# Optimization experiments

Measured on AMD Instinct MI355X. Metric: run time of the kernel, lower is better.

The kernel has to match this reference:

```python
import jax, jax.numpy as jnp
import numpy as np

HID, SD, EXP, DTR = 1024, 16, 2048, 64
B_, T_ = 4, 2048


def setup_inputs() -> dict:
    key = jax.random.key(0)
    ks = jax.random.split(key, 9)
    def rn(k, shape, s=0.02):
        return jax.random.normal(k, shape, jnp.float32) * s
    return {
        "x": jax.random.normal(ks[0], (B_, T_, HID), jnp.float32),
        "ln_g": jnp.ones((HID,), jnp.float32),
        "ln_b": jnp.zeros((HID,), jnp.float32),
        "W_in": rn(ks[1], (HID, 2 * EXP)),
        "b_in": jnp.zeros((2 * EXP,), jnp.float32),
        "W_del": rn(ks[2], (EXP, DTR)),
        "b_del": jnp.zeros((DTR,), jnp.float32),
        "W_dt": rn(ks[3], (DTR, EXP)),
        "b_dt": jnp.zeros((EXP,), jnp.float32),
        "W_B": rn(ks[4], (EXP, SD)),
        "b_B": jnp.zeros((SD,), jnp.float32),
        "W_C": rn(ks[5], (EXP, SD)),
        "b_C": jnp.zeros((SD,), jnp.float32),
        "A_log": -jnp.exp(0.1 * jax.random.normal(ks[6], (EXP, SD), jnp.float32)),
        "Dp": jnp.zeros((EXP,), jnp.float32),
        "W_out": rn(ks[7], (EXP, HID)),
        "b_out": jnp.zeros((HID,), jnp.float32),
    }


def _layernorm(x, g, b, eps=1e-5):
    m = jnp.mean(x, axis=-1, keepdims=True)
    v = jnp.var(x, axis=-1, keepdims=True)
    return (x - m) * jax.lax.rsqrt(v + eps) * g + b


def _selective_scan(u, delta, A, Bm, Cm):
    # u, delta: (B,T,E); Bm, Cm: (B,T,Sd); A: (E,Sd)
    def step(h, inp):
        u_t, d_t, B_t, C_t = inp  # (B,E),(B,E),(B,Sd),(B,Sd)
        A_disc = jnp.exp(d_t[..., None] * A[None])          # (B,E,Sd)
        h = A_disc * h + d_t[..., None] * B_t[:, None, :] * u_t[..., None]
        y_t = jnp.einsum("bs,bds->bd", C_t, h)
        return h, y_t
    h0 = jnp.zeros((u.shape[0], u.shape[2], A.shape[1]), u.dtype)
    xs = (u.transpose(1, 0, 2), delta.transpose(1, 0, 2),
          Bm.transpose(1, 0, 2), Cm.transpose(1, 0, 2))
    _, ys = jax.lax.scan(step, h0, xs)  # ys: (T,B,E)
    return ys.transpose(1, 0, 2)


def reference(x, ln_g, ln_b, W_in, b_in, W_del, b_del, W_dt, b_dt,
              W_B, b_B, W_C, b_C, A_log, Dp, W_out, b_out):
    res = x
    xn = _layernorm(x, ln_g, ln_b)
    xp = xn @ W_in + b_in                 # (B,T,2E)
    u, gate = jnp.split(xp, 2, axis=-1)   # each (B,T,E)
    u = jax.nn.silu(u)
    delta = jax.nn.softplus((u @ W_del + b_del) @ W_dt + b_dt)  # (B,T,E)
    Bm = u @ W_B + b_B                    # (B,T,Sd)
    Cm = u @ W_C + b_C                    # (B,T,Sd)
    A = -jnp.exp(A_log)                   # (E,Sd)
    y = _selective_scan(u, delta, A, Bm, Cm)
    y = y + u * Dp
    y = y * jax.nn.silu(gate)
    return y @ W_out + b_out + res
```

## Files before the change

kernel.cpp:

```cpp
#include <hip/hip_runtime.h>

#define HIDN 1024
#define EXPN 2048
#define SDIM 16
#define DTRN 64
#define BBN  4
#define TTN  2048
#define MMN  (BBN*TTN)
#define NCHUNK 64
#define CLEN (TTN/NCHUNK)
#define KSPL 4
#define KCH  (EXPN/KSPL)

typedef unsigned short u16;
typedef __bf16 bf16x8 __attribute__((ext_vector_type(8)));
typedef float f32x4 __attribute__((ext_vector_type(4)));
typedef float f32x2v __attribute__((ext_vector_type(2)));

static __device__ __forceinline__ float b2f(u16 u) {
    union { unsigned int i; float f; } cv; cv.i = ((unsigned int)u) << 16; return cv.f;
}
static __device__ __forceinline__ u16 f2b(float f) {
    union { float f; unsigned int i; } cv; cv.f = f;
    unsigned int x = cv.i;
    return (u16)((x + 0x7fffu + ((x >> 16) & 1u)) >> 16);
}
static __device__ __forceinline__ float fexp2(float x) {
    return __builtin_amdgcn_exp2f(x);
}
static __device__ __forceinline__ float fsilu(float v) {
    return v / (1.f + fexp2(-1.44269504088896f * v));
}
template<int L> static __device__ __forceinline__ void waitcnt_vm() {
    if constexpr (L == 0) asm volatile("s_waitcnt vmcnt(0)" ::: "memory");
    else if constexpr (L == 3) asm volatile("s_waitcnt vmcnt(3)" ::: "memory");
    else if constexpr (L == 4) asm volatile("s_waitcnt vmcnt(4)" ::: "memory");
}

static __device__ __forceinline__
void tr_tile(const float* __restrict__ W, u16* __restrict__ Wt,
             int K, int N, int bk, int bn, float (*t)[65]) {
    const int r0 = threadIdx.x >> 4, c0 = (threadIdx.x & 15) << 2;
    #pragma unroll
    for (int i = 0; i < 4; ++i) {
        float4 v = *(const float4*)(W + (size_t)(bk + r0 + i * 16) * N + bn + c0);
        t[r0 + i * 16][c0 + 0] = v.x; t[r0 + i * 16][c0 + 1] = v.y;
        t[r0 + i * 16][c0 + 2] = v.z; t[r0 + i * 16][c0 + 3] = v.w;
    }
    __syncthreads();
    #pragma unroll
    for (int i = 0; i < 4; ++i) {
        const int n = r0 + i * 16;
        ushort4 o;
        o.x = f2b(t[c0 + 0][n]); o.y = f2b(t[c0 + 1][n]);
        o.z = f2b(t[c0 + 2][n]); o.w = f2b(t[c0 + 3][n]);
        *(ushort4*)(Wt + (size_t)(bn + n) * K + bk + c0) = o;
    }
}

__global__ __launch_bounds__(256)
void k_prep(const float* __restrict__ x, const float* __restrict__ ln_g,
            const float* __restrict__ ln_b,
            const float* __restrict__ W_in, const float* __restrict__ W_out,
            const float* __restrict__ W_dt, const float* __restrict__ W_del,
            const float* __restrict__ W_B, const float* __restrict__ W_C,
            const float* __restrict__ A_log,
            u16* __restrict__ xn,
            u16* __restrict__ Wt_in, u16* __restrict__ Wt_out,
            u16* __restrict__ Wdt_t, u16* __restrict__ Wcat,
            float* __restrict__ A2) {
    __shared__ float t[64][65];
    __shared__ float as[4], bs[4];
    int blk = blockIdx.x;
    if (blk < MMN) {
        const int row = blk, tid = threadIdx.x;
        const float4 xv = ((const float4*)(x + (size_t)row * HIDN))[tid];
        float s  = xv.x + xv.y + xv.z + xv.w;
        float ss = fmaf(xv.x, xv.x, fmaf(xv.y, xv.y, fmaf(xv.z, xv.z, xv.w * xv.w)));
        #pragma unroll
        for (int o = 32; o > 0; o >>= 1) { s += __shfl_down(s, o); ss += __shfl_down(ss, o); }
        const int wid = tid >> 6, lane = tid & 63;
        if (lane == 0) { as[wid] = s; bs[wid] = ss; }
        __syncthreads();
        const float S  = as[0] + as[1] + as[2] + as[3];
        const float SS = bs[0] + bs[1] + bs[2] + bs[3];
        const float mean = S * (1.f / HIDN);
        const float var  = SS * (1.f / HIDN) - mean * mean;
        const float r = rsqrtf(var + 1e-5f);
        const float4 gv = ((const float4*)ln_g)[tid];
        const float4 bv = ((const float4*)ln_b)[tid];
        ushort4 o;
        o.x = f2b((xv.x - mean) * r * gv.x + bv.x);
        o.y = f2b((xv.y - mean) * r * gv.y + bv.y);
        o.z = f2b((xv.z - mean) * r * gv.z + bv.z);
        o.w = f2b((xv.w - mean) * r * gv.w + bv.w);
        ((ushort4*)(xn + (size_t)row * HIDN))[tid] = o;
        return;
    }
    blk -= MMN;
    if (blk < 1024) {
        tr_tile(W_in, Wt_in, HIDN, 2 * EXPN, (blk >> 6) << 6, (blk & 63) << 6, t);
        return;
    }
    blk -= 1024;
    if (blk < 512) {
        tr_tile(W_out, Wt_out, EXPN, HIDN, (blk >> 4) << 6, (blk & 15) << 6, t);
        return;
    }
    blk -= 512;
    if (blk < 32) {
        tr_tile(W_dt, Wdt_t, DTRN, EXPN, 0, blk << 6, t);
        return;
    }
    blk -= 32;
    if (blk < 768) {
        const int i = blk * 256 + threadIdx.x;
        const int n = i >> 11, k = i & 2047;
        float v;
        if (n < 64)      v = W_del[(size_t)k * DTRN + n];
        else if (n < 80) v = W_B[(size_t)k * SDIM + (n - 64)];
        else             v = W_C[(size_t)k * SDIM + (n - 80)];
        Wcat[i] = f2b(v);
        return;
    }
    blk -= 768;
    {
        const int i = blk * 256 + threadIdx.x;
        A2[i] = -__expf(A_log[i]) * 1.44269504088896340736f;
    }
}

#define MEPI_SPLIT_SILU 0
#define MEPI_OUT        1
#define MEPI_SP         2

template<int BN>
static __device__ __forceinline__
void stage256(const u16* __restrict__ A, const u16* __restrict__ Bt,
              u16 (*seg)[8192], int brow, int bcol, int K, int k0,
              int srow, int scol, int tid) {
    #pragma unroll
    for (int h = 0; h < 2; ++h) {
        const u16* sa = A + (size_t)(brow + h * 128 + srow) * K + k0 + scol;
        __builtin_amdgcn_global_load_lds(
            (const __attribute__((address_space(1))) void*)sa,
            (__attribute__((address_space(3))) void*)&seg[h][tid * 8], 16, 0, 0);
    }
    #pragma unroll
    for (int h = 0; h < BN / 128; ++h) {
        const u16* sb = Bt + (size_t)(bcol + h * 128 + srow) * K + k0 + scol;
        __builtin_amdgcn_global_load_lds(
            (const __attribute__((address_space(1))) void*)sb,
            (__attribute__((address_space(3))) void*)&seg[2 + h][tid * 8], 16, 0, 0);
    }
}

template<int BN, int EPI>
__global__ __launch_bounds__(1024)
void mgemm256(const u16* __restrict__ A, const u16* __restrict__ Bt,
              const float* __restrict__ bias, void* __restrict__ O0,
              void* __restrict__ O1, const float* __restrict__ res,
              int N, int K) {
    constexpr int NSEG = 2 + BN / 128;
    constexpr int L    = NSEG;
    constexpr int NFRag = BN / 64;
    __shared__ u16 lds[2][NSEG][8192];
    const int tid  = threadIdx.x;
    const int lane = tid & 63, wid = tid >> 6;
    const int wm = wid >> 2, wn = wid & 3;
    const int r  = lane & 15, kh = lane >> 4;
    const int brow = blockIdx.y * 256, bcol = blockIdx.x * BN;

    int srow, scol;
    {
        const int q = tid;
        const int sub = q >> 6, qi = q & 63;
        const int qis = qi ^ (((qi >> 5) & 1) << 1);
        srow = (sub >> 1) * 16 + (qi >> 2);
        scol = ((sub & 1) << 5) + (qis & 3) * 8;
    }
    const int swz_kh = kh ^ (((r >> 3) & 1) << 1);
    const int rbase  = r * 32 + swz_kh * 8;
    const int am = wm & 1;

    f32x4 acc[4][NFRag];
    #pragma unroll
    for (int i = 0; i < 4; ++i)
        #pragma unroll
        for (int n = 0; n < NFRag; ++n) acc[i][n] = (f32x4){0.f, 0.f, 0.f, 0.f};

    const int NT = K >> 6;
    stage256<BN>(A, Bt, lds[0], brow, bcol, K, 0, srow, scol, tid);
    if (NT > 1) {
        stage256<BN>(A, Bt, lds[1], brow, bcol, K, 64, srow, scol, tid);
        waitcnt_vm<L>();
    } else {
        waitcnt_vm<0>();
    }
    __builtin_amdgcn_s_barrier();
    asm volatile("" ::: "memory");

    for (int kt = 0; kt < NT; ++kt) {
        const u16* segA = lds[kt & 1][wm >> 1];
        #pragma unroll
        for (int kk = 0; kk < 2; ++kk) {
            bf16x8 a[4], b[NFRag];
            #pragma unroll
            for (int mf = 0; mf < 4; ++mf)
                a[mf] = *(const bf16x8*)&segA[((am * 4 + mf) * 2 + kk) * 512 + rbase];
            #pragma unroll
            for (int nf = 0; nf < NFRag; ++nf) {
                const int nb = wn * NFRag + nf;
                const u16* segB = lds[kt & 1][2 + (nb >> 3)];
                b[nf] = *(const bf16x8*)&segB[(((nb & 7)) * 2 + kk) * 512 + rbase];
            }
            __builtin_amdgcn_s_setprio(1);
            #pragma unroll
            for (int mf = 0; mf < 4; ++mf)
                #pragma unroll
                for (int nf = 0; nf < NFRag; ++nf)
                    acc[mf][nf] = __builtin_amdgcn_mfma_f32_16x16x32_bf16(a[mf], b[nf], acc[mf][nf], 0, 0, 0);
            __builtin_amdgcn_s_setprio(0);
        }
        __builtin_amdgcn_s_barrier(); asm volatile("" ::: "memory");
        if (kt + 2 < NT) {
            stage256<BN>(A, Bt, lds[kt & 1], brow, bcol, K, (kt + 2) * 64, srow, scol, tid);
            waitcnt_vm<L>();
        } else {
            waitcnt_vm<0>();
        }
        __builtin_amdgcn_s_barrier(); asm volatile("" ::: "memory");
    }

    const int orow = brow + wm * 64 + kh * 4;
    const int ocol = bcol + wn * (BN / 4) + r;
    if constexpr (EPI == MEPI_SPLIT_SILU) {
        u16* dst; int cb;
        if (bcol < EXPN) { dst = (u16*)O0; cb = ocol; }
        else             { dst = (u16*)O1; cb = ocol - EXPN; }
        #pragma unroll
        for (int Mf = 0; Mf < 4; ++Mf)
            #pragma unroll
            for (int Nf = 0; Nf < NFRag; ++Nf)
                #pragma unroll
                for (int j = 0; j < 4; ++j) {
                    const int row = orow + Mf * 16 + j;
                    const int col = ocol + Nf * 16;
                    float v = acc[Mf][Nf][j] + bias[col];
                    dst[(size_t)row * EXPN + cb + Nf * 16] = f2b(fsilu(v));
                }
    } else if constexpr (EPI == MEPI_SP) {
        u16* o = (u16*)O0;
        #pragma unroll
        for (int Mf = 0; Mf < 4; ++Mf)
            #pragma unroll
            for (int Nf = 0; Nf < NFRag; ++Nf)
                #pragma unroll
                for (int j = 0; j < 4; ++j) {
                    const int row = orow + Mf * 16 + j;
                    const int col = ocol + Nf * 16;
                    float v = acc[Mf][Nf][j] + bias[col];
                    float sp = (v > 20.f) ? v
                             : 0.69314718056f * __builtin_amdgcn_logf(
                                   1.f + fexp2(1.44269504089f * v));
                    o[(size_t)row * N + col] = f2b(sp);
                }
    } else {
        float* o = (float*)O0;
        #pragma unroll
        for (int Mf = 0; Mf < 4; ++Mf)
            #pragma unroll
            for (int Nf = 0; Nf < NFRag; ++Nf)
                #pragma unroll
                for (int j = 0; j < 4; ++j) {
                    const int row = orow + Mf * 16 + j;
                    const int col = ocol + Nf * 16;
                    o[(size_t)row * N + col] = acc[Mf][Nf][j] + bias[col] + res[(size_t)row * N + col];
                }
    }
}

__global__ __launch_bounds__(256)
void k_proj(const u16* __restrict__ A, const u16* __restrict__ Wcat,
            float* __restrict__ Ppart) {
    __shared__ u16 As[128 * 32];
    __shared__ u16 Bs[96 * 32];
    const int tid  = threadIdx.x;
    const int wave = tid >> 6, lane = tid & 63;
    const int brow = blockIdx.y * 128;
    const int ks   = blockIdx.x;
    const int r = lane & 15, kh = lane >> 4;

    f32x4 acc[2][6];
    #pragma unroll
    for (int m = 0; m < 2; m++)
        #pragma unroll
        for (int n = 0; n < 6; n++) acc[m][n] = (f32x4){0.f, 0.f, 0.f, 0.f};

    const u16* ga0 = A + (size_t)(brow +      (tid >> 2)) * EXPN + ks * KCH + (tid & 3) * 8;
    const u16* ga1 = A + (size_t)(brow + 64 + (tid >> 2)) * EXPN + ks * KCH + (tid & 3) * 8;
    const u16* gb0 = Wcat + (size_t)(tid >> 2) * EXPN + ks * KCH + (tid & 3) * 8;
    const u16* gb1 = Wcat + (size_t)(64 + (tid >> 2)) * EXPN + ks * KCH + (tid & 3) * 8;
    u16* lA0 = As + (wave * 64) * 8;
    u16* lA1 = As + (256 + wave * 64) * 8;
    u16* lB0 = Bs + (wave * 64) * 8;
    u16* lB1 = Bs + (256 + wave * 64) * 8;

    for (int k0 = 0; k0 < KCH; k0 += 32) {
        __syncthreads();
        __builtin_amdgcn_global_load_lds((const __attribute__((address_space(1))) void*)(ga0 + k0),
                                         (__attribute__((address_space(3))) void*)lA0, 16, 0, 0);
        __builtin_amdgcn_global_load_lds((const __attribute__((address_space(1))) void*)(ga1 + k0),
                                         (__attribute__((address_space(3))) void*)lA1, 16, 0, 0);
        __builtin_amdgcn_global_load_lds((const __attribute__((address_space(1))) void*)(gb0 + k0),
                                         (__attribute__((address_space(3))) void*)lB0, 16, 0, 0);
        if (tid < 128)
            __builtin_amdgcn_global_load_lds((const __attribute__((address_space(1))) void*)(gb1 + k0),
                                             (__attribute__((address_space(3))) void*)lB1, 16, 0, 0);
        __syncthreads();
        bf16x8 af[2], bfr[6];
        #pragma unroll
        for (int mf = 0; mf < 2; ++mf)
            af[mf] = *(const bf16x8*)(As + ((wave * 32 + mf * 16 + r) * 32 + kh * 8));
        #pragma unroll
        for (int nf = 0; nf < 6; ++nf)
            bfr[nf] = *(const bf16x8*)(Bs + ((nf * 16 + r) * 32 + kh * 8));
        #pragma unroll
        for (int mf = 0; mf < 2; ++mf)
            #pragma unroll
            for (int nf = 0; nf < 6; ++nf)
                acc[mf][nf] = __builtin_amdgcn_mfma_f32_16x16x32_bf16(af[mf], bfr[nf], acc[mf][nf], 0, 0, 0);
    }
    const int orow = brow + wave * 32 + kh * 4;
    #pragma unroll
    for (int mf = 0; mf < 2; ++mf)
        #pragma unroll
        for (int nf = 0; nf < 6; ++nf)
            #pragma unroll
            for (int j = 0; j < 4; ++j)
                Ppart[((size_t)ks * MMN + orow + mf * 16 + j) * 96 + nf * 16 + r] = acc[mf][nf][j];
}

__global__ __launch_bounds__(192)
void k_red(const float* __restrict__ Ppart, const float* __restrict__ b_del,
           const float* __restrict__ b_B, const float* __restrict__ b_C,
           u16* __restrict__ t1b, float* __restrict__ Bm, float* __restrict__ Cm) {
    const int tid = threadIdx.x;
    const int ri  = tid / 96, col = tid - ri * 96;
    const int row = blockIdx.x * 2 + ri;
    float s = 0.f;
    #pragma unroll
    for (int ks = 0; ks < KSPL; ++ks)
        s += Ppart[((size_t)ks * MMN + row) * 96 + col];
    if (col < 64)      t1b[(size_t)row * DTRN + col] = f2b(s + b_del[col]);
    else if (col < 80) Bm[(size_t)row * SDIM + col - 64] = s + b_B[col - 64];
    else               Cm[(size_t)row * SDIM + col - 80] = s + b_C[col - 80];
}

__global__ __launch_bounds__(256)
void k_scan1(const u16* __restrict__ ub, const u16* __restrict__ db,
             const float* __restrict__ Bm, const float* __restrict__ A2,
             u16* __restrict__ hend, u16* __restrict__ Pp) {
    const int e = blockIdx.x * 256 + threadIdx.x;
    const int c = blockIdx.y, b = blockIdx.z;
    f32x2v a2p[8], hp[8];
    {
        const float4* ap = (const float4*)(A2 + (size_t)e * SDIM);
        #pragma unroll
        for (int q = 0; q < 4; ++q) {
            float4 v = ap[q];
            a2p[2*q]   = (f32x2v){v.x, v.y};
            a2p[2*q+1] = (f32x2v){v.z, v.w};
        }
    }
    #pragma unroll
    for (int i = 0; i < 8; ++i) hp[i] = (f32x2v){0.f, 0.f};
    float sumd = 0.f;
    const int t0 = c * CLEN;
    size_t rb = ((size_t)b * TTN + t0) * EXPN + e;
    size_t bb_ = ((size_t)b * TTN + t0) * SDIM;
    float dC = b2f(db[rb]), uC = b2f(ub[rb]);
    for (int tt = 0; tt < CLEN; ++tt) {
        const float dN = b2f(db[rb + EXPN]);
        const float uN = b2f(ub[rb + EXPN]);
        const float4* bp = (const float4*)(Bm + bb_);
        f32x2v bvp[8];
        #pragma unroll
        for (int q = 0; q < 4; ++q) {
            float4 v = bp[q];
            bvp[2*q]   = (f32x2v){v.x, v.y};
            bvp[2*q+1] = (f32x2v){v.z, v.w};
        }
        const float du = dC * uC;
        sumd += dC;
        #pragma unroll
        for (int i = 0; i < 8; ++i) {
            f32x2v arg = a2p[i] * dC;
            f32x2v ad; ad.x = fexp2(arg.x); ad.y = fexp2(arg.y);
            hp[i] = ad * hp[i] + bvp[i] * du;
        }
        dC = dN; uC = uN;
        rb += EXPN; bb_ += SDIM;
    }
    const size_t base = ((size_t)((b * NCHUNK + c)) * EXPN + e) * 16;
    union { u16 s[16]; uint4 v[2]; } he, pv;
    #pragma unroll
    for (int i = 0; i < 8; ++i) {
        he.s[2*i]   = f2b(hp[i].x);
        he.s[2*i+1] = f2b(hp[i].y);
        pv.s[2*i]   = f2b(fexp2(a2p[i].x * sumd));
        pv.s[2*i+1] = f2b(fexp2(a2p[i].y * sumd));
    }
    *(uint4*)(hend + base)     = he.v[0];
    *(uint4*)(hend + base + 8) = he.v[1];
    *(uint4*)(Pp + base)       = pv.v[0];
    *(uint4*)(Pp + base + 8)   = pv.v[1];
}

__global__ __launch_bounds__(256)
void k_fix(const u16* __restrict__ hend, const u16* __restrict__ Pp,
           u16* __restrict__ hinit) {
    const int i = blockIdx.x * 256 + threadIdx.x;
    const int b = blockIdx.y;
    float hi = 0.f;
    size_t idx = (size_t)b * NCHUNK * (EXPN * 16) + i;
    u16 pC = Pp[idx], hC = hend[idx];
    for (int cc = 0; cc < NCHUNK; ++cc) {
        const size_t idx2 = idx + EXPN * 16;
        u16 pN = 0, hN = 0;
        if (cc + 1 < NCHUNK) { pN = Pp[idx2]; hN = hend[idx2]; }
        hinit[idx] = f2b(hi);
        hi = fmaf(b2f(pC), hi, b2f(hC));
        pC = pN; hC = hN; idx = idx2;
    }
}

__global__ __launch_bounds__(256)
void k_scan2(const u16* __restrict__ ub, const u16* __restrict__ db,
             const u16* __restrict__ sgb, const float* __restrict__ Bm,
             const float* __restrict__ Cm, const float* __restrict__ A2,
             const u16* __restrict__ hinit, const float* __restrict__ Dp,
             u16* __restrict__ yb) {
    const int e = blockIdx.x * 256 + threadIdx.x;
    const int c = blockIdx.y, b = blockIdx.z;
    f32x2v a2p[8], hp[8];
    {
        const float4* ap = (const float4*)(A2 + (size_t)e * SDIM);
        #pragma unroll
        for (int q = 0; q < 4; ++q) {
            float4 v = ap[q];
            a2p[2*q]   = (f32x2v){v.x, v.y};
            a2p[2*q+1] = (f32x2v){v.z, v.w};
        }
    }
    {
        const size_t base = ((size_t)((b * NCHUNK + c)) * EXPN + e) * 16;
        union { u16 s[16]; uint4 v[2]; } hi;
        hi.v[0] = *(const uint4*)(hinit + base);
        hi.v[1] = *(const uint4*)(hinit + base + 8);
        #pragma unroll
        for (int i = 0; i < 8; ++i)
            hp[i] = (f32x2v){b2f(hi.s[2*i]), b2f(hi.s[2*i+1])};
    }
    const float dpe = Dp[e];
    const int t0 = c * CLEN;
    size_t rb = ((size_t)b * TTN + t0) * EXPN + e;
    size_t bb_ = ((size_t)b * TTN + t0) * SDIM;
    float dC = b2f(db[rb]), uC = b2f(ub[rb]), gC = b2f(sgb[rb]);
    for (int tt = 0; tt < CLEN; ++tt) {
        const float dN = b2f(db[rb + EXPN]);
        const float uN = b2f(ub[rb + EXPN]);
        const float gN = b2f(sgb[rb + EXPN]);
        const float4* bp = (const float4*)(Bm + bb_);
        const float4* cp = (const float4*)(Cm + bb_);
        f32x2v bvp[8], cvp[8];
        #pragma unroll
        for (int q = 0; q < 4; ++q) {
            float4 v = bp[q];
            bvp[2*q]   = (f32x2v){v.x, v.y};
            bvp[2*q+1] = (f32x2v){v.z, v.w};
            float4 w = cp[q];
            cvp[2*q]   = (f32x2v){w.x, w.y};
            cvp[2*q+1] = (f32x2v){w.z, w.w};
        }
        const float du = dC * uC;
        f32x2v ytp = (f32x2v){0.f, 0.f};
        #pragma unroll
        for (int i = 0; i < 8; ++i) {
            f32x2v arg = a2p[i] * dC;
            f32x2v ad; ad.x = fexp2(arg.x); ad.y = fexp2(arg.y);
            hp[i] = ad * hp[i] + bvp[i] * du;
            ytp = ytp + cvp[i] * hp[i];
        }
        yb[rb] = f2b(fmaf(uC, dpe, ytp.x + ytp.y) * gC);
        dC = dN; uC = uN; gC = gN;
        rb += EXPN; bb_ += SDIM;
    }
}

extern "C" void kernel_launch(void* const* d_in, const int* in_sizes, int n_in,
                              void* d_out, int out_size, void* d_ws, size_t ws_size,
                              hipStream_t stream) {
    const float* x     = (const float*)d_in[0];
    const float* ln_g  = (const float*)d_in[1];
    const float* ln_b  = (const float*)d_in[2];
    const float* W_in  = (const float*)d_in[3];
    const float* b_in  = (const float*)d_in[4];
    const float* W_del = (const float*)d_in[5];
    const float* b_del = (const float*)d_in[6];
    const float* W_dt  = (const float*)d_in[7];
    const float* b_dt  = (const float*)d_in[8];
    const float* W_B   = (const float*)d_in[9];
    const float* b_B   = (const float*)d_in[10];
    const float* W_C   = (const float*)d_in[11];
    const float* b_C   = (const float*)d_in[12];
    const float* A_log = (const float*)d_in[13];
    const float* Dp    = (const float*)d_in[14];
    const float* W_out = (const float*)d_in[15];
    const float* b_out = (const float*)d_in[16];
    float* out = (float*)d_out;

    char* p = (char*)d_ws;
    auto alloc = [&](size_t bytes) {
        char* r = p; p += (bytes + 255) & ~(size_t)255; return (void*)r;
    };
    u16* xn   = (u16*)alloc((size_t)MMN * HIDN * 2);
    u16* u    = (u16*)alloc((size_t)MMN * EXPN * 2);
    u16* sg   = (u16*)alloc((size_t)MMN * EXPN * 2);
    u16* dl   = (u16*)alloc((size_t)MMN * EXPN * 2);
    u16* y    = (u16*)alloc((size_t)MMN * EXPN * 2);
    u16* t1b  = (u16*)alloc((size_t)MMN * DTRN * 2);
    float* Bm = (float*)alloc((size_t)MMN * SDIM * 4);
    float* Cm = (float*)alloc((size_t)MMN * SDIM * 4);
    float* A2 = (float*)alloc((size_t)EXPN * SDIM * 4);
    u16* Wt_in  = (u16*)alloc((size_t)(2 * EXPN) * HIDN * 2);
    u16* Wt_out = (u16*)alloc((size_t)HIDN * EXPN * 2);
    u16* Wcat   = (u16*)alloc((size_t)96 * EXPN * 2);
    u16* Wdt_t  = (u16*)alloc((size_t)EXPN * DTRN * 2);
    const size_t hsz = (size_t)BBN * NCHUNK * EXPN * SDIM * 2;
    u16* hend  = (u16*)alloc(hsz);
    u16* Pp    = (u16*)alloc(hsz);
    u16* hinit = (u16*)alloc(hsz);
    float* Ppart = (float*)hend;

    k_prep<<<dim3(MMN + 1024 + 512 + 32 + 768 + 128), 256, 0, stream>>>(
        x, ln_g, ln_b, W_in, W_out, W_dt, W_del, W_B, W_C, A_log,
        xn, Wt_in, Wt_out, Wdt_t, Wcat, A2);

    mgemm256<256, MEPI_SPLIT_SILU><<<dim3(2 * EXPN / 256, MMN / 256), 1024, 0, stream>>>(
        xn, Wt_in, b_in, u, sg, nullptr, 2 * EXPN, HIDN);
    k_proj<<<dim3(KSPL, MMN / 128), 256, 0, stream>>>(u, Wcat, Ppart);
    k_red<<<dim3(MMN / 2), 192, 0, stream>>>(Ppart, b_del, b_B, b_C, t1b, Bm, Cm);
    mgemm256<128, MEPI_SP><<<dim3(EXPN / 128, MMN / 256), 1024, 0, stream>>>(
        t1b, Wdt_t, b_dt, dl, nullptr, nullptr, EXPN, DTRN);
    k_scan1<<<dim3(EXPN / 256, NCHUNK, BBN), 256, 0, stream>>>(u, dl, Bm, A2, hend, Pp);
    k_fix<<<dim3(EXPN * SDIM / 256, BBN), 256, 0, stream>>>(hend, Pp, hinit);
    k_scan2<<<dim3(EXPN / 256, NCHUNK, BBN), 256, 0, stream>>>(u, dl, sg, Bm, Cm, A2, hinit, Dp, y);
    mgemm256<128, MEPI_OUT><<<dim3(HIDN / 128, MMN / 256), 1024, 0, stream>>>(
        y, Wt_out, b_out, out, nullptr, x, HIDN, EXPN);
}
```

Before: 284.6 us.

## Fuse split-K reduction into k_proj via last-block atomic counter; swizzle GEMM blocks

The separate k_red launch is removed. Each k_proj row-block now increments an atomic counter after a threadfence, and the last of the KSPL split-K blocks sums the partials and writes t1b, Bm and Cm. A counter buffer is zeroed with hipMemsetAsync each call. Separately, mgemm256 remaps block indices with an XCD-style round-robin swizzle so that neighbouring tiles share L2 on the same die. The reduction adds serialized tail work in the last block and an extra memset launch.

New measurement: 352.5 us. +23.9%, slower.

```diff
diff --git a/kernel.cpp b/kernel.cpp
--- a/kernel.cpp
+++ b/kernel.cpp
@@ -169,7 +169,11 @@
     const int lane = tid & 63, wid = tid >> 6;
     const int wm = wid >> 2, wn = wid & 3;
     const int r  = lane & 15, kh = lane >> 4;
-    const int brow = blockIdx.y * 256, bcol = blockIdx.x * BN;
+    const int nwg  = gridDim.x * gridDim.y;
+    const int orig = blockIdx.y * gridDim.x + blockIdx.x;
+    const int swz  = (orig & 7) * (nwg >> 3) + (orig >> 3);
+    const int bx   = swz % gridDim.x, by = swz / gridDim.x;
+    const int brow = by * 256, bcol = bx * BN;
 
     int srow, scol;
     {
@@ -282,7 +286,11 @@
 
 __global__ __launch_bounds__(256)
 void k_proj(const u16* __restrict__ A, const u16* __restrict__ Wcat,
-            float* __restrict__ Ppart) {
+            float* __restrict__ Ppart, unsigned int* __restrict__ cnt,
+            const float* __restrict__ b_del, const float* __restrict__ b_B,
+            const float* __restrict__ b_C,
+            u16* __restrict__ t1b, float* __restrict__ Bm,
+            float* __restrict__ Cm) {
     __shared__ u16 As[128 * 32];
     __shared__ u16 Bs[96 * 32];
     const int tid  = threadIdx.x;
@@ -339,22 +347,25 @@
             #pragma unroll
             for (int j = 0; j < 4; ++j)
                 Ppart[((size_t)ks * MMN + orow + mf * 16 + j) * 96 + nf * 16 + r] = acc[mf][nf][j];
-}
-
-__global__ __launch_bounds__(192)
-void k_red(const float* __restrict__ Ppart, const float* __restrict__ b_del,
-           const float* __restrict__ b_B, const float* __restrict__ b_C,
-           u16* __restrict__ t1b, float* __restrict__ Bm, float* __restrict__ Cm) {
-    const int tid = threadIdx.x;
-    const int ri  = tid / 96, col = tid - ri * 96;
-    const int row = blockIdx.x * 2 + ri;
-    float s = 0.f;
-    #pragma unroll
-    for (int ks = 0; ks < KSPL; ++ks)
-        s += Ppart[((size_t)ks * MMN + row) * 96 + col];
-    if (col < 64)      t1b[(size_t)row * DTRN + col] = f2b(s + b_del[col]);
-    else if (col < 80) Bm[(size_t)row * SDIM + col - 64] = s + b_B[col - 64];
-    else               Cm[(size_t)row * SDIM + col - 80] = s + b_C[col - 80];
+
+    __threadfence();
+    __syncthreads();
+    __shared__ unsigned int last;
+    if (tid == 0) last = atomicAdd(&cnt[blockIdx.y], 1u);
+    __syncthreads();
+    if (last != KSPL - 1) return;
+    __threadfence();
+    for (int it = tid; it < 128 * 96; it += 256) {
+        const int row = brow + it / 96;
+        const int col = it % 96;
+        float s = 0.f;
+        #pragma unroll
+        for (int k = 0; k < KSPL; ++k)
+            s += Ppart[((size_t)k * MMN + row) * 96 + col];
+        if (col < 64)      t1b[(size_t)row * DTRN + col] = f2b(s + b_del[col]);
+        else if (col < 80) Bm[(size_t)row * SDIM + col - 64] = s + b_B[col - 64];
+        else               Cm[(size_t)row * SDIM + col - 80] = s + b_C[col - 80];
+    }
 }
 
 __global__ __launch_bounds__(256)
@@ -537,20 +548,23 @@
     u16* Wt_out = (u16*)alloc((size_t)HIDN * EXPN * 2);
     u16* Wcat   = (u16*)alloc((size_t)96 * EXPN * 2);
     u16* Wdt_t  = (u16*)alloc((size_t)EXPN * DTRN * 2);
+    unsigned int* cnt = (unsigned int*)alloc(256 * sizeof(unsigned int));
     const size_t hsz = (size_t)BBN * NCHUNK * EXPN * SDIM * 2;
     u16* hend  = (u16*)alloc(hsz);
     u16* Pp    = (u16*)alloc(hsz);
     u16* hinit = (u16*)alloc(hsz);
     float* Ppart = (float*)hend;
 
+    hipMemsetAsync(cnt, 0, 256 * sizeof(unsigned int), stream);
+
     k_prep<<<dim3(MMN + 1024 + 512 + 32 + 768 + 128), 256, 0, stream>>>(
         x, ln_g, ln_b, W_in, W_out, W_dt, W_del, W_B, W_C, A_log,
         xn, Wt_in, Wt_out, Wdt_t, Wcat, A2);
 
     mgemm256<256, MEPI_SPLIT_SILU><<<dim3(2 * EXPN / 256, MMN / 256), 1024, 0, stream>>>(
         xn, Wt_in, b_in, u, sg, nullptr, 2 * EXPN, HIDN);
-    k_proj<<<dim3(KSPL, MMN / 128), 256, 0, stream>>>(u, Wcat, Ppart);
-    k_red<<<dim3(MMN / 2), 192, 0, stream>>>(Ppart, b_del, b_B, b_C, t1b, Bm, Cm);
+    k_proj<<<dim3(KSPL, MMN / 128), 256, 0, stream>>>(
+        u, Wcat, Ppart, cnt, b_del, b_B, b_C, t1b, Bm, Cm);
     mgemm256<128, MEPI_SP><<<dim3(EXPN / 128, MMN / 256), 1024, 0, stream>>>(
         t1b, Wdt_t, b_dt, dl, nullptr, nullptr, EXPN, DTRN);
     k_scan1<<<dim3(EXPN / 256, NCHUNK, BBN), 256, 0, stream>>>(u, dl, Bm, A2, hend, Pp);
```
